# Kernel tuning notes

Measured on AMD Instinct MI355X. Metric: run time of the kernel, lower is better.

Reference implementation:

```python
import jax, jax.numpy as jnp
import numpy as np

N = 100000
E = 1600000
NODE_DIM = 8
HIDDEN = 32
N_ACTIONS = 3


def _glorot(key, shape):
    fan_in, fan_out = shape[0], shape[1]
    lim = (6.0 / (fan_in + fan_out)) ** 0.5
    return jax.random.uniform(key, shape, jnp.float32, -lim, lim)


def setup_inputs() -> dict:
    key = jax.random.key(0)
    ks = jax.random.split(key, 16)
    x = jax.random.normal(ks[0], (N, NODE_DIM), jnp.float32)
    edge_index = jax.random.randint(ks[1], (2, E), 0, N, jnp.int64)
    # SAGEConv params: lin_l (aggregated neighbors, with bias), lin_r (root, no bias)
    params = {}
    dims = [(NODE_DIM, HIDDEN), (HIDDEN, HIDDEN), (HIDDEN, HIDDEN)]
    for i, (din, dout) in enumerate(dims, start=1):
        params[f"Wl{i}"] = _glorot(ks[2 * i], (din, dout))
        params[f"bl{i}"] = jnp.zeros((dout,), jnp.float32)
        params[f"Wr{i}"] = _glorot(ks[2 * i + 1], (din, dout))
    # MLP head
    params["Wh1"] = _glorot(ks[10], (HIDDEN, HIDDEN))
    params["bh1"] = jnp.zeros((HIDDEN,), jnp.float32)
    params["Wh2"] = _glorot(ks[11], (HIDDEN, N_ACTIONS))
    params["bh2"] = jnp.zeros((N_ACTIONS,), jnp.float32)
    return {"x": x, "edge_index": edge_index, **params}


def _sage_conv(x, src, dst, Wl, bl, Wr):
    # mean-aggregate neighbor features at each target node
    msg_sum = jax.ops.segment_sum(x[src], dst, num_segments=N)  # [N, d]
    deg = jax.ops.segment_sum(jnp.ones((src.shape[0],), x.dtype), dst, num_segments=N)
    mean = msg_sum / jnp.maximum(deg, 1.0)[:, None]
    return mean @ Wl + bl + x @ Wr


def reference(x, edge_index, Wl1, bl1, Wr1, Wl2, bl2, Wr2, Wl3, bl3, Wr3, Wh1, bh1, Wh2, bh2):
    src, dst = edge_index[0], edge_index[1]
    h = jax.nn.relu(_sage_conv(x, src, dst, Wl1, bl1, Wr1))
    h = jax.nn.relu(_sage_conv(h, src, dst, Wl2, bl2, Wr2))
    h = jax.nn.relu(_sage_conv(h, src, dst, Wl3, bl3, Wr3))
    h = jax.nn.relu(h @ Wh1 + bh1)
    return h @ Wh2 + bh2  # [N, n_actions]
```

## Files before the change

kernel.cpp:

```cpp
#include <hip/hip_runtime.h>
#include <hip/hip_bf16.h>

#define NN 100000
#define NE 1600000
#define DIN 8
#define DH 32
#define NACT 3
#define NBLK 391
#define PADN (NBLK * 256)
#define BKN 128
#define NBKT 782
#define CAPB 3072
#define PA 128
#define ECA (NE / PA)
#define LG32 (NN / 32)

typedef __hip_bfloat16 bf;
typedef unsigned short u16;
typedef __attribute__((ext_vector_type(8))) short bf16x8;
typedef __attribute__((ext_vector_type(4))) float f32x4;

__device__ __forceinline__ float bflo(unsigned u) { return __uint_as_float(u << 16); }
__device__ __forceinline__ float bfhi(unsigned u) { return __uint_as_float(u & 0xffff0000u); }
__device__ __forceinline__ unsigned pk2(float lo, float hi) {
    union { bf b; unsigned short u; } cl, ch;
    cl.b = __float2bfloat16(lo); ch.b = __float2bfloat16(hi);
    return (unsigned)cl.u | ((unsigned)ch.u << 16);
}

__launch_bounds__(256)
__global__ void prep_weights(const float* __restrict__ Wl1, const float* __restrict__ Wr1,
                             const float* __restrict__ Wl2, const float* __restrict__ Wr2,
                             const float* __restrict__ Wl3, const float* __restrict__ Wr3,
                             const float* __restrict__ Wh1,
                             u16* __restrict__ B1t, u16* __restrict__ B2t,
                             u16* __restrict__ B3t, u16* __restrict__ Bh1t) {
    int tid = threadIdx.x;
    for (int idx = tid; idx < 1024; idx += 256) {
        int j = idx >> 5, k = idx & 31;
        float v = (k < 8) ? Wl1[k * DH + j] : ((k < 16) ? Wr1[(k - 8) * DH + j] : 0.0f);
        reinterpret_cast<bf*>(B1t)[j * 32 + k] = __float2bfloat16(v);
    }
    for (int idx = tid; idx < 2048; idx += 256) {
        int j = idx >> 6, k = idx & 63;
        float v = (k < 32) ? Wl2[k * DH + j] : Wr2[(k - 32) * DH + j];
        reinterpret_cast<bf*>(B2t)[j * 64 + k] = __float2bfloat16(v);
    }
    for (int idx = tid; idx < 2048; idx += 256) {
        int j = idx >> 6, k = idx & 63;
        float v = (k < 32) ? Wl3[k * DH + j] : Wr3[(k - 32) * DH + j];
        reinterpret_cast<bf*>(B3t)[j * 64 + k] = __float2bfloat16(v);
    }
    for (int idx = tid; idx < 1024; idx += 256) {
        int j = idx >> 5, k = idx & 31;
        reinterpret_cast<bf*>(Bh1t)[j * 32 + k] = __float2bfloat16(Wh1[k * DH + j]);
    }
}

__launch_bounds__(256)
__global__ void partition_edges(const int* __restrict__ src, const int* __restrict__ dst,
                                int* __restrict__ bucket_cnt, unsigned* __restrict__ ebuf) {
    __shared__ int lcnt[NBKT];
    __shared__ int lbase[NBKT];
    int tid = threadIdx.x;
    for (int r = tid; r < NBKT; r += 256) lcnt[r] = 0;
    __syncthreads();

    int e0 = blockIdx.x * ECA;
    for (int e = e0 + tid * 4; e < e0 + ECA; e += 1024) {
        int4 d4 = *reinterpret_cast<const int4*>(&dst[e]);
        atomicAdd(&lcnt[(unsigned)d4.x >> 7], 1);
        atomicAdd(&lcnt[(unsigned)d4.y >> 7], 1);
        atomicAdd(&lcnt[(unsigned)d4.z >> 7], 1);
        atomicAdd(&lcnt[(unsigned)d4.w >> 7], 1);
    }
    __syncthreads();
    for (int r = tid; r < NBKT; r += 256) {
        lbase[r] = atomicAdd(&bucket_cnt[r], lcnt[r]);
        lcnt[r] = 0;
    }
    __syncthreads();
    for (int e = e0 + tid * 4; e < e0 + ECA; e += 1024) {
        int4 d4 = *reinterpret_cast<const int4*>(&dst[e]);
        int4 s4 = *reinterpret_cast<const int4*>(&src[e]);
        int r, p;
        r = (unsigned)d4.x >> 7; p = lbase[r] + atomicAdd(&lcnt[r], 1);
        if (p < CAPB) ebuf[r * CAPB + p] = ((unsigned)s4.x << 7) | ((unsigned)d4.x & 127u);
        r = (unsigned)d4.y >> 7; p = lbase[r] + atomicAdd(&lcnt[r], 1);
        if (p < CAPB) ebuf[r * CAPB + p] = ((unsigned)s4.y << 7) | ((unsigned)d4.y & 127u);
        r = (unsigned)d4.z >> 7; p = lbase[r] + atomicAdd(&lcnt[r], 1);
        if (p < CAPB) ebuf[r * CAPB + p] = ((unsigned)s4.z << 7) | ((unsigned)d4.z & 127u);
        r = (unsigned)d4.w >> 7; p = lbase[r] + atomicAdd(&lcnt[r], 1);
        if (p < CAPB) ebuf[r * CAPB + p] = ((unsigned)s4.w << 7) | ((unsigned)d4.w & 127u);
    }
}

__launch_bounds__(256)
__global__ void count_local(const int* __restrict__ bucket_cnt,
                            const unsigned* __restrict__ ebuf, int* __restrict__ degI) {
    __shared__ int cnt[BKN];
    int tid = threadIdx.x;
    int r = blockIdx.x;
    if (tid < BKN) cnt[tid] = 0;
    __syncthreads();
    int n = min(bucket_cnt[r], CAPB);
    const unsigned* eb = ebuf + r * CAPB;
    for (int i = tid; i < n; i += 256)
        atomicAdd(&cnt[eb[i] & 127u], 1);
    __syncthreads();
    int node = r * BKN + tid;
    if (tid < BKN && node < NN) degI[node] = cnt[tid];
}

__launch_bounds__(256)
__global__ void scanA(const int* __restrict__ degI, int* __restrict__ incl,
                      int* __restrict__ bsum) {
    __shared__ int s[256];
    int i = blockIdx.x * 256 + threadIdx.x;
    int v = (i < NN) ? degI[i] : 0;
    s[threadIdx.x] = v;
    __syncthreads();
#pragma unroll
    for (int off = 1; off < 256; off <<= 1) {
        int t = (threadIdx.x >= off) ? s[threadIdx.x - off] : 0;
        __syncthreads();
        s[threadIdx.x] += t;
        __syncthreads();
    }
    incl[i] = s[threadIdx.x];
    if (threadIdx.x == 255) bsum[blockIdx.x] = s[255];
}

__launch_bounds__(512)
__global__ void scanB(int* __restrict__ bsum) {
    __shared__ int s[512];
    int tid = threadIdx.x;
    int v = (tid < NBLK) ? bsum[tid] : 0;
    s[tid] = v;
    __syncthreads();
#pragma unroll
    for (int off = 1; off < 512; off <<= 1) {
        int t = (tid >= off) ? s[tid - off] : 0;
        __syncthreads();
        s[tid] += t;
        __syncthreads();
    }
    if (tid < NBLK) bsum[tid] = s[tid] - v;
}

__launch_bounds__(256)
__global__ void scanC(const int* __restrict__ incl, const int* __restrict__ degI,
                      const int* __restrict__ bsum, int* __restrict__ start) {
    int i = blockIdx.x * 256 + threadIdx.x;
    if (i < NN)
        start[i] = incl[i] - degI[i] + bsum[blockIdx.x];
}

__launch_bounds__(256)
__global__ void fill_local(const int* __restrict__ bucket_cnt,
                           const unsigned* __restrict__ ebuf,
                           const int* __restrict__ start, int* __restrict__ adj) {
    __shared__ int lcur[BKN];
    __shared__ int sstart[BKN];
    int tid = threadIdx.x;
    int r = blockIdx.x;
    if (tid < BKN) {
        lcur[tid] = 0;
        int node = r * BKN + tid;
        sstart[tid] = (node < NN) ? start[node] : 0;
    }
    __syncthreads();
    int n = min(bucket_cnt[r], CAPB);
    const unsigned* eb = ebuf + r * CAPB;
    for (int i = tid; i < n; i += 256) {
        unsigned v = eb[i];
        int d = v & 127u;
        int pos = atomicAdd(&lcur[d], 1);
        adj[sstart[d] + pos] = (int)(v >> 7);
    }
}

__launch_bounds__(128)
__global__ void layer1_mfma(const float* __restrict__ x, const int* __restrict__ degI,
                            const int* __restrict__ start, const int* __restrict__ adj,
                            const u16* __restrict__ Bt, const float* __restrict__ blv,
                            bf* __restrict__ hout) {
    __shared__ __align__(16) short sA[32 * 72];
    int tid = threadIdx.x;
    int base = blockIdx.x * 32;

    {
        int row = tid >> 2, part = tid & 3;
        *reinterpret_cast<uint2*>(&sA[row * 72 + 16 + part * 4]) = make_uint2(0u, 0u);
    }

    int g = tid >> 5, t = tid & 31;
    int nb = t >> 1, q = t & 1;
    int nbase = base + g * 8;
    int dgv = 0, stv = 0;
    if (t < 8) { dgv = degI[nbase + t]; stv = start[nbase + t]; }

#pragma unroll 4
    for (int i = 0; i < 8; ++i) {
        int dg  = __shfl(dgv, i, 32);
        int row = __shfl(stv, i, 32);
        int node = nbase + i;
        int idxreg = (t < dg) ? adj[row + t] : 0;
        float4 xv;
        if (t == 2 || t == 3)
            xv = *reinterpret_cast<const float4*>(&x[node * DIN + (t - 2) * 4]);
        float a[4] = {0.f, 0.f, 0.f, 0.f};
        int lim = min(dg, 32);
        int nit = (lim + 15) >> 4;
        for (int j = 0; j < nit; ++j) {
            int k = nb + j * 16;
            int s = __shfl(idxreg, k, 32);
            float4 v = *reinterpret_cast<const float4*>(&x[s * DIN + q * 4]);
            if (k < lim) { a[0] += v.x; a[1] += v.y; a[2] += v.z; a[3] += v.w; }
        }
        for (int k = 32 + nb; k < dg; k += 16) {
            int s = adj[row + k];
            float4 v = *reinterpret_cast<const float4*>(&x[s * DIN + q * 4]);
            a[0] += v.x; a[1] += v.y; a[2] += v.z; a[3] += v.w;
        }
#pragma unroll
        for (int m = 0; m < 4; ++m) {
            a[m] += __shfl_xor(a[m], 2);
            a[m] += __shfl_xor(a[m], 4);
            a[m] += __shfl_xor(a[m], 8);
            a[m] += __shfl_xor(a[m], 16);
        }
        int nrow = g * 8 + i;
        if (t < 2) {
            float inv = 1.0f / fmaxf((float)dg, 1.0f);
            uint2 mm;
            mm.x = pk2(a[0] * inv, a[1] * inv);
            mm.y = pk2(a[2] * inv, a[3] * inv);
            *reinterpret_cast<uint2*>(&sA[nrow * 72 + t * 4]) = mm;
        } else if (t < 4) {
            uint2 xm;
            xm.x = pk2(xv.x, xv.y);
            xm.y = pk2(xv.z, xv.w);
            *reinterpret_cast<uint2*>(&sA[nrow * 72 + 8 + (t - 2) * 4]) = xm;
        }
    }
    __syncthreads();

    int wid = tid >> 6, lane = tid & 63;
    int r16 = lane & 15, k8 = (lane >> 4) * 8;
    bf16x8 av = *reinterpret_cast<const bf16x8*>(&sA[(wid * 16 + r16) * 72 + k8]);
    bf16x8 b0 = *reinterpret_cast<const bf16x8*>(&Bt[r16 * 32 + k8]);
    bf16x8 b1 = *reinterpret_cast<const bf16x8*>(&Bt[(16 + r16) * 32 + k8]);
    f32x4 acc0 = {0.f, 0.f, 0.f, 0.f}, acc1 = {0.f, 0.f, 0.f, 0.f};
    acc0 = __builtin_amdgcn_mfma_f32_16x16x32_bf16(av, b0, acc0, 0, 0, 0);
    acc1 = __builtin_amdgcn_mfma_f32_16x16x32_bf16(av, b1, acc1, 0, 0, 0);
    float bias0 = blv[r16], bias1 = blv[16 + r16];
    int rbase = base + wid * 16 + (lane >> 4) * 4;
#pragma unroll
    for (int reg = 0; reg < 4; ++reg) {
        int node = rbase + reg;
        hout[node * DH + r16]      = __float2bfloat16(fmaxf(acc0[reg] + bias0, 0.f));
        hout[node * DH + 16 + r16] = __float2bfloat16(fmaxf(acc1[reg] + bias1, 0.f));
    }
}

__device__ __forceinline__ void gather32(const bf* __restrict__ hin,
                                         const int* __restrict__ degI,
                                         const int* __restrict__ start,
                                         const int* __restrict__ adj,
                                         short* sA, int base, int tid) {
    int g = tid >> 5, t = tid & 31;
    int nb = t >> 2, q = t & 3;
    int nbase = base + g * 8;
    int dgv = 0, stv = 0;
    if (t < 8) { dgv = degI[nbase + t]; stv = start[nbase + t]; }

#pragma unroll 4
    for (int i = 0; i < 8; ++i) {
        int dg  = __shfl(dgv, i, 32);
        int row = __shfl(stv, i, 32);
        int node = nbase + i;
        int idxreg = (t < dg) ? adj[row + t] : 0;
        uint4 xru;
        if ((t & 28) == 4)
            xru = *reinterpret_cast<const uint4*>(&hin[node * DH + (t - 4) * 8]);
        float a[8] = {0.f, 0.f, 0.f, 0.f, 0.f, 0.f, 0.f, 0.f};
        int lim = min(dg, 32);
        int nit = (lim + 7) >> 3;
        for (int j = 0; j < nit; ++j) {
            int k = nb + j * 8;
            int s = __shfl(idxreg, k, 32);
            uint4 u = *reinterpret_cast<const uint4*>(&hin[s * DH + q * 8]);
            if (k < lim) {
                a[0] += bflo(u.x); a[1] += bfhi(u.x);
                a[2] += bflo(u.y); a[3] += bfhi(u.y);
                a[4] += bflo(u.z); a[5] += bfhi(u.z);
                a[6] += bflo(u.w); a[7] += bfhi(u.w);
            }
        }
        for (int k = 32 + nb; k < dg; k += 8) {
            int s = adj[row + k];
            uint4 u = *reinterpret_cast<const uint4*>(&hin[s * DH + q * 8]);
            a[0] += bflo(u.x); a[1] += bfhi(u.x);
            a[2] += bflo(u.y); a[3] += bfhi(u.y);
            a[4] += bflo(u.z); a[5] += bfhi(u.z);
            a[6] += bflo(u.w); a[7] += bfhi(u.w);
        }
#pragma unroll
        for (int m = 0; m < 8; ++m) {
            a[m] += __shfl_xor(a[m], 4);
            a[m] += __shfl_xor(a[m], 8);
            a[m] += __shfl_xor(a[m], 16);
        }
        int nrow = g * 8 + i;
        if (t < 4) {
            float inv = 1.0f / fmaxf((float)dg, 1.0f);
            uint4 mm;
            mm.x = pk2(a[0] * inv, a[1] * inv);
            mm.y = pk2(a[2] * inv, a[3] * inv);
            mm.z = pk2(a[4] * inv, a[5] * inv);
            mm.w = pk2(a[6] * inv, a[7] * inv);
            *reinterpret_cast<uint4*>(&sA[nrow * 72 + t * 8]) = mm;
        } else if (t < 8) {
            *reinterpret_cast<uint4*>(&sA[nrow * 72 + 32 + (t - 4) * 8]) = xru;
        }
    }
}

__launch_bounds__(128)
__global__ void layer2_mfma(const bf* __restrict__ hin, const int* __restrict__ degI,
                            const int* __restrict__ start, const int* __restrict__ adj,
                            const u16* __restrict__ Bt, const float* __restrict__ blv,
                            bf* __restrict__ hout) {
    __shared__ __align__(16) short sA[32 * 72];
    int tid = threadIdx.x;
    int base = blockIdx.x * 32;

    gather32(hin, degI, start, adj, sA, base, tid);
    __syncthreads();

    int wid = tid >> 6, lane = tid & 63;
    int r16 = lane & 15, k8 = (lane >> 4) * 8;
    const short* ap = &sA[(wid * 16 + r16) * 72];
    bf16x8 av0 = *reinterpret_cast<const bf16x8*>(&ap[k8]);
    bf16x8 av1 = *reinterpret_cast<const bf16x8*>(&ap[32 + k8]);
    const u16* b0p = &Bt[r16 * 64];
    const u16* b1p = &Bt[(16 + r16) * 64];
    bf16x8 b00 = *reinterpret_cast<const bf16x8*>(&b0p[k8]);
    bf16x8 b01 = *reinterpret_cast<const bf16x8*>(&b0p[32 + k8]);
    bf16x8 b10 = *reinterpret_cast<const bf16x8*>(&b1p[k8]);
    bf16x8 b11 = *reinterpret_cast<const bf16x8*>(&b1p[32 + k8]);
    f32x4 acc0 = {0.f, 0.f, 0.f, 0.f}, acc1 = {0.f, 0.f, 0.f, 0.f};
    acc0 = __builtin_amdgcn_mfma_f32_16x16x32_bf16(av0, b00, acc0, 0, 0, 0);
    acc0 = __builtin_amdgcn_mfma_f32_16x16x32_bf16(av1, b01, acc0, 0, 0, 0);
    acc1 = __builtin_amdgcn_mfma_f32_16x16x32_bf16(av0, b10, acc1, 0, 0, 0);
    acc1 = __builtin_amdgcn_mfma_f32_16x16x32_bf16(av1, b11, acc1, 0, 0, 0);
    float bias0 = blv[r16], bias1 = blv[16 + r16];
    int rbase = base + wid * 16 + (lane >> 4) * 4;
#pragma unroll
    for (int reg = 0; reg < 4; ++reg) {
        int node = rbase + reg;
        hout[node * DH + r16]      = __float2bfloat16(fmaxf(acc0[reg] + bias0, 0.f));
        hout[node * DH + 16 + r16] = __float2bfloat16(fmaxf(acc1[reg] + bias1, 0.f));
    }
}

__launch_bounds__(128)
__global__ void layer3_mfma(const bf* __restrict__ hin, const int* __restrict__ degI,
                            const int* __restrict__ start, const int* __restrict__ adj,
                            const u16* __restrict__ B3t, const float* __restrict__ bl3,
                            const u16* __restrict__ Bh1t, const float* __restrict__ bh1,
                            const float* __restrict__ Wh2, const float* __restrict__ bh2,
                            float* __restrict__ out) {
    __shared__ __align__(16) short sA[32 * 72];
    __shared__ float sW2[NACT * DH];
    int tid = threadIdx.x;
    int base = blockIdx.x * 32;

    if (tid < NACT * DH) {
        int a = tid >> 5, k = tid & 31;
        sW2[a * DH + k] = Wh2[k * NACT + a];
    }

    gather32(hin, degI, start, adj, sA, base, tid);
    __syncthreads();

    int wid = tid >> 6, lane = tid & 63;
    int r16 = lane & 15, k8 = (lane >> 4) * 8;
    int rloc = wid * 16 + (lane >> 4) * 4;

    f32x4 acc0 = {0.f, 0.f, 0.f, 0.f}, acc1 = {0.f, 0.f, 0.f, 0.f};
    {
        const short* ap = &sA[(wid * 16 + r16) * 72];
        bf16x8 av0 = *reinterpret_cast<const bf16x8*>(&ap[k8]);
        bf16x8 av1 = *reinterpret_cast<const bf16x8*>(&ap[32 + k8]);
        const u16* b0p = &B3t[r16 * 64];
        const u16* b1p = &B3t[(16 + r16) * 64];
        bf16x8 b00 = *reinterpret_cast<const bf16x8*>(&b0p[k8]);
        bf16x8 b01 = *reinterpret_cast<const bf16x8*>(&b0p[32 + k8]);
        bf16x8 b10 = *reinterpret_cast<const bf16x8*>(&b1p[k8]);
        bf16x8 b11 = *reinterpret_cast<const bf16x8*>(&b1p[32 + k8]);
        acc0 = __builtin_amdgcn_mfma_f32_16x16x32_bf16(av0, b00, acc0, 0, 0, 0);
        acc0 = __builtin_amdgcn_mfma_f32_16x16x32_bf16(av1, b01, acc0, 0, 0, 0);
        acc1 = __builtin_amdgcn_mfma_f32_16x16x32_bf16(av0, b10, acc1, 0, 0, 0);
        acc1 = __builtin_amdgcn_mfma_f32_16x16x32_bf16(av1, b11, acc1, 0, 0, 0);
    }
    __syncthreads();

    bf* h3b = reinterpret_cast<bf*>(sA);
    {
        float bias0 = bl3[r16], bias1 = bl3[16 + r16];
#pragma unroll
        for (int reg = 0; reg < 4; ++reg) {
            int rr = rloc + reg;
            h3b[rr * 40 + r16]      = __float2bfloat16(fmaxf(acc0[reg] + bias0, 0.f));
            h3b[rr * 40 + 16 + r16] = __float2bfloat16(fmaxf(acc1[reg] + bias1, 0.f));
        }
    }
    __syncthreads();

    f32x4 d0 = {0.f, 0.f, 0.f, 0.f}, d1 = {0.f, 0.f, 0.f, 0.f};
    {
        bf16x8 av = *reinterpret_cast<const bf16x8*>(&h3b[(wid * 16 + r16) * 40 + k8]);
        bf16x8 b0 = *reinterpret_cast<const bf16x8*>(&Bh1t[r16 * 32 + k8]);
        bf16x8 b1 = *reinterpret_cast<const bf16x8*>(&Bh1t[(16 + r16) * 32 + k8]);
        d0 = __builtin_amdgcn_mfma_f32_16x16x32_bf16(av, b0, d0, 0, 0, 0);
        d1 = __builtin_amdgcn_mfma_f32_16x16x32_bf16(av, b1, d1, 0, 0, 0);
    }
    __syncthreads();

    float* shm = reinterpret_cast<float*>(sA);
    {
        float hb0 = bh1[r16], hb1 = bh1[16 + r16];
#pragma unroll
        for (int reg = 0; reg < 4; ++reg) {
            int rr = rloc + reg;
            shm[rr * 36 + r16]      = fmaxf(d0[reg] + hb0, 0.f);
            shm[rr * 36 + 16 + r16] = fmaxf(d1[reg] + hb1, 0.f);
        }
    }
    __syncthreads();

    {
        int m = tid >> 2, a = tid & 3;
        if (a < NACT) {
            float o = bh2[a];
            const float* hp = &shm[m * 36];
            const float* wp = &sW2[a * DH];
#pragma unroll
            for (int k = 0; k < DH; k += 4) {
                f32x4 hv = *reinterpret_cast<const f32x4*>(&hp[k]);
                f32x4 wv = *reinterpret_cast<const f32x4*>(&wp[k]);
                o += hv.x * wv.x + hv.y * wv.y + hv.z * wv.z + hv.w * wv.w;
            }
            out[(base + m) * NACT + a] = o;
        }
    }
}

extern "C" void kernel_launch(void* const* d_in, const int* in_sizes, int n_in,
                              void* d_out, int out_size, void* d_ws, size_t ws_size,
                              hipStream_t stream) {
    const float* x   = (const float*)d_in[0];
    const int*   ei  = (const int*)d_in[1];
    const int*   src = ei;
    const int*   dst = ei + NE;
    const float* Wl1 = (const float*)d_in[2];
    const float* bl1 = (const float*)d_in[3];
    const float* Wr1 = (const float*)d_in[4];
    const float* Wl2 = (const float*)d_in[5];
    const float* bl2 = (const float*)d_in[6];
    const float* Wr2 = (const float*)d_in[7];
    const float* Wl3 = (const float*)d_in[8];
    const float* bl3 = (const float*)d_in[9];
    const float* Wr3 = (const float*)d_in[10];
    const float* Wh1 = (const float*)d_in[11];
    const float* bh1 = (const float*)d_in[12];
    const float* Wh2 = (const float*)d_in[13];
    const float* bh2 = (const float*)d_in[14];
    float* out = (float*)d_out;

    int* degI      = (int*)d_ws;
    int* bucket    = degI + NN;
    int* startP    = bucket + NBKT;
    int* bsum      = startP + NN;
    int* incl      = bsum + 512;
    int* adj       = incl + PADN;
    unsigned* ebuf = (unsigned*)(adj + NE);
    u16* B1t       = (u16*)(ebuf + NBKT * CAPB);
    u16* B2t       = B1t + 1024;
    u16* B3t       = B2t + 2048;
    u16* Bh1t      = B3t + 2048;
    bf*  hA        = (bf*)(Bh1t + 1024);
    bf*  hB        = hA + DH * NN;

    hipMemsetAsync(degI, 0, (NN + NBKT) * sizeof(int), stream);

    prep_weights<<<1, 256, 0, stream>>>(Wl1, Wr1, Wl2, Wr2, Wl3, Wr3, Wh1,
                                        B1t, B2t, B3t, Bh1t);

    partition_edges<<<PA, 256, 0, stream>>>(src, dst, bucket, ebuf);
    count_local<<<NBKT, 256, 0, stream>>>(bucket, ebuf, degI);
    scanA<<<NBLK, 256, 0, stream>>>(degI, incl, bsum);
    scanB<<<1, 512, 0, stream>>>(bsum);
    scanC<<<NBLK, 256, 0, stream>>>(incl, degI, bsum, startP);
    fill_local<<<NBKT, 256, 0, stream>>>(bucket, ebuf, startP, adj);

    layer1_mfma<<<LG32, 128, 0, stream>>>(x, degI, startP, adj, B1t, bl1, hA);
    layer2_mfma<<<LG32, 128, 0, stream>>>(hA, degI, startP, adj, B2t, bl2, hB);
    layer3_mfma<<<LG32, 128, 0, stream>>>(hB, degI, startP, adj, B3t, bl3,
                                          Bh1t, bh1, Wh2, bh2, out);
}
```

Measured before the change: 228.0 us.

## Replace per-node degree scan with bucket-level scan and fused CSR fill

The separate count, three-stage node prefix scan and fill kernels are replaced by a single-block scan over bucket counts plus one fused kernel per bucket. The fused kernel stages the bucket's edges in shared memory, counts degrees, does a local prefix scan, then writes degI, startP and the adjacency. This removes several launches, a second global read of ebuf and the node-level scan traffic, and shrinks the memset. The cost is a larger shared-memory footprint per block (about 12KB), which may lower occupancy.

```diff
diff --git a/kernel.cpp b/kernel.cpp
--- a/kernel.cpp
+++ b/kernel.cpp
@@ -6,8 +6,6 @@
 #define DIN 8
 #define DH 32
 #define NACT 3
-#define NBLK 391
-#define PADN (NBLK * 256)
 #define BKN 128
 #define NBKT 782
 #define CAPB 3072
@@ -96,87 +94,75 @@
 }
 
 __launch_bounds__(256)
-__global__ void count_local(const int* __restrict__ bucket_cnt,
-                            const unsigned* __restrict__ ebuf, int* __restrict__ degI) {
-    __shared__ int cnt[BKN];
-    int tid = threadIdx.x;
-    int r = blockIdx.x;
-    if (tid < BKN) cnt[tid] = 0;
-    __syncthreads();
-    int n = min(bucket_cnt[r], CAPB);
-    const unsigned* eb = ebuf + r * CAPB;
-    for (int i = tid; i < n; i += 256)
-        atomicAdd(&cnt[eb[i] & 127u], 1);
-    __syncthreads();
-    int node = r * BKN + tid;
-    if (tid < BKN && node < NN) degI[node] = cnt[tid];
-}
-
-__launch_bounds__(256)
-__global__ void scanA(const int* __restrict__ degI, int* __restrict__ incl,
-                      int* __restrict__ bsum) {
+__global__ void scan_buckets(const int* __restrict__ bucket_cnt, int* __restrict__ bucket_base) {
     __shared__ int s[256];
-    int i = blockIdx.x * 256 + threadIdx.x;
-    int v = (i < NN) ? degI[i] : 0;
-    s[threadIdx.x] = v;
+    int tid = threadIdx.x;
+    int i0 = tid * 4;
+    int v0 = (i0 + 0 < NBKT) ? min(bucket_cnt[i0 + 0], CAPB) : 0;
+    int v1 = (i0 + 1 < NBKT) ? min(bucket_cnt[i0 + 1], CAPB) : 0;
+    int v2 = (i0 + 2 < NBKT) ? min(bucket_cnt[i0 + 2], CAPB) : 0;
+    int v3 = (i0 + 3 < NBKT) ? min(bucket_cnt[i0 + 3], CAPB) : 0;
+    s[tid] = v0 + v1 + v2 + v3;
     __syncthreads();
 #pragma unroll
     for (int off = 1; off < 256; off <<= 1) {
-        int t = (threadIdx.x >= off) ? s[threadIdx.x - off] : 0;
-        __syncthreads();
-        s[threadIdx.x] += t;
-        __syncthreads();
-    }
-    incl[i] = s[threadIdx.x];
-    if (threadIdx.x == 255) bsum[blockIdx.x] = s[255];
-}
-
-__launch_bounds__(512)
-__global__ void scanB(int* __restrict__ bsum) {
-    __shared__ int s[512];
-    int tid = threadIdx.x;
-    int v = (tid < NBLK) ? bsum[tid] : 0;
-    s[tid] = v;
-    __syncthreads();
-#pragma unroll
-    for (int off = 1; off < 512; off <<= 1) {
         int t = (tid >= off) ? s[tid - off] : 0;
         __syncthreads();
         s[tid] += t;
         __syncthreads();
     }
-    if (tid < NBLK) bsum[tid] = s[tid] - v;
+    int prev = (tid > 0) ? s[tid - 1] : 0;
+    if (i0 + 0 < NBKT) bucket_base[i0 + 0] = prev;
+    if (i0 + 1 < NBKT) bucket_base[i0 + 1] = prev + v0;
+    if (i0 + 2 < NBKT) bucket_base[i0 + 2] = prev + v0 + v1;
+    if (i0 + 3 < NBKT) bucket_base[i0 + 3] = prev + v0 + v1 + v2;
 }
 
 __launch_bounds__(256)
-__global__ void scanC(const int* __restrict__ incl, const int* __restrict__ degI,
-                      const int* __restrict__ bsum, int* __restrict__ start) {
-    int i = blockIdx.x * 256 + threadIdx.x;
-    if (i < NN)
-        start[i] = incl[i] - degI[i] + bsum[blockIdx.x];
-}
-
-__launch_bounds__(256)
-__global__ void fill_local(const int* __restrict__ bucket_cnt,
+__global__ void fill_fused(const int* __restrict__ bucket_cnt, const int* __restrict__ bucket_base,
                            const unsigned* __restrict__ ebuf,
-                           const int* __restrict__ start, int* __restrict__ adj) {
-    __shared__ int lcur[BKN];
-    __shared__ int sstart[BKN];
+                           int* __restrict__ degI, int* __restrict__ startP,
+                           int* __restrict__ adj) {
+    __shared__ unsigned sc[CAPB];
+    __shared__ int cnt[BKN];
+    __shared__ int lofs[BKN];
+    __shared__ int cur[BKN];
     int tid = threadIdx.x;
     int r = blockIdx.x;
-    if (tid < BKN) {
-        lcur[tid] = 0;
-        int node = r * BKN + tid;
-        sstart[tid] = (node < NN) ? start[node] : 0;
-    }
-    __syncthreads();
     int n = min(bucket_cnt[r], CAPB);
+    if (tid < BKN) { cnt[tid] = 0; cur[tid] = 0; }
+    __syncthreads();
     const unsigned* eb = ebuf + r * CAPB;
     for (int i = tid; i < n; i += 256) {
         unsigned v = eb[i];
+        sc[i] = v;
+        atomicAdd(&cnt[v & 127u], 1);
+    }
+    __syncthreads();
+    if (tid < BKN) lofs[tid] = cnt[tid];
+    __syncthreads();
+#pragma unroll
+    for (int off = 1; off < BKN; off <<= 1) {
+        int t = 0;
+        if (tid < BKN && tid >= off) t = lofs[tid - off];
+        __syncthreads();
+        if (tid < BKN) lofs[tid] += t;
+        __syncthreads();
+    }
+    if (tid < BKN) lofs[tid] -= cnt[tid];
+    __syncthreads();
+    int gbase = bucket_base[r];
+    int node = r * BKN + tid;
+    if (tid < BKN && node < NN) {
+        degI[node]   = cnt[tid];
+        startP[node] = gbase + lofs[tid];
+    }
+    __syncthreads();
+    for (int i = tid; i < n; i += 256) {
+        unsigned v = sc[i];
         int d = v & 127u;
-        int pos = atomicAdd(&lcur[d], 1);
-        adj[sstart[d] + pos] = (int)(v >> 7);
+        int p = atomicAdd(&cur[d], 1);
+        adj[gbase + lofs[d] + p] = (int)(v >> 7);
     }
 }
 
@@ -480,31 +466,27 @@
     const float* bh2 = (const float*)d_in[14];
     float* out = (float*)d_out;
 
-    int* degI      = (int*)d_ws;
-    int* bucket    = degI + NN;
-    int* startP    = bucket + NBKT;
-    int* bsum      = startP + NN;
-    int* incl      = bsum + 512;
-    int* adj       = incl + PADN;
-    unsigned* ebuf = (unsigned*)(adj + NE);
-    u16* B1t       = (u16*)(ebuf + NBKT * CAPB);
-    u16* B2t       = B1t + 1024;
-    u16* B3t       = B2t + 2048;
-    u16* Bh1t      = B3t + 2048;
-    bf*  hA        = (bf*)(Bh1t + 1024);
-    bf*  hB        = hA + DH * NN;
-
-    hipMemsetAsync(degI, 0, (NN + NBKT) * sizeof(int), stream);
+    int* bucket      = (int*)d_ws;
+    int* bucket_base = bucket + NBKT;
+    int* degI        = bucket_base + NBKT;
+    int* startP      = degI + NN;
+    int* adj         = startP + NN;
+    unsigned* ebuf   = (unsigned*)(adj + NE);
+    u16* B1t         = (u16*)(ebuf + NBKT * CAPB);
+    u16* B2t         = B1t + 1024;
+    u16* B3t         = B2t + 2048;
+    u16* Bh1t        = B3t + 2048;
+    bf*  hA          = (bf*)(Bh1t + 1024);
+    bf*  hB          = hA + DH * NN;
+
+    hipMemsetAsync(bucket, 0, NBKT * sizeof(int), stream);
 
     prep_weights<<<1, 256, 0, stream>>>(Wl1, Wr1, Wl2, Wr2, Wl3, Wr3, Wh1,
                                         B1t, B2t, B3t, Bh1t);
 
     partition_edges<<<PA, 256, 0, stream>>>(src, dst, bucket, ebuf);
-    count_local<<<NBKT, 256, 0, stream>>>(bucket, ebuf, degI);
-    scanA<<<NBLK, 256, 0, stream>>>(degI, incl, bsum);
-    scanB<<<1, 512, 0, stream>>>(bsum);
-    scanC<<<NBLK, 256, 0, stream>>>(incl, degI, bsum, startP);
-    fill_local<<<NBKT, 256, 0, stream>>>(bucket, ebuf, startP, adj);
+    scan_buckets<<<1, 256, 0, stream>>>(bucket, bucket_base);
+    fill_fused<<<NBKT, 256, 0, stream>>>(bucket, bucket_base, ebuf, degI, startP, adj);
 
     layer1_mfma<<<LG32, 128, 0, stream>>>(x, degI, startP, adj, B1t, bl1, hA);
     layer2_mfma<<<LG32, 128, 0, stream>>>(hA, degI, startP, adj, B2t, bl2, hB);
```

Result: faster. 222.5 us (-2.4%).
